# Kernel tuning notes

Hardware: AMD Instinct MI355X
Metric: run time of the kernel (lower is better)

Reference implementation:

```python
import jax, jax.numpy as jnp
import numpy as np

HIDDEN = 4096
N_HEADS = 32
N_KV_HEADS = 8
HEAD_DIM = HIDDEN // N_HEADS  # 128
Q_BITS = 8
ROPE_BASE = 10000.0


def setup_inputs() -> dict:
    key = jax.random.key(0)
    ks = jax.random.split(key, 6)
    b, s = 1, 2048
    hidden_states = jax.random.normal(ks[0], (b, s, HIDDEN), dtype=jnp.float32)
    position_ids = jnp.arange(s, dtype=jnp.int64 if jax.config.jax_enable_x64 else jnp.int32)[None, :]
    w_scale = 0.02
    wq = jax.random.normal(ks[1], (N_HEADS * HEAD_DIM, HIDDEN), dtype=jnp.float32) * w_scale
    wk = jax.random.normal(ks[2], (N_KV_HEADS * HEAD_DIM, HIDDEN), dtype=jnp.float32) * w_scale
    wv = jax.random.normal(ks[3], (N_KV_HEADS * HEAD_DIM, HIDDEN), dtype=jnp.float32) * w_scale
    wo = jax.random.normal(ks[4], (HIDDEN, N_HEADS * HEAD_DIM), dtype=jnp.float32) * w_scale
    return {"hidden_states": hidden_states, "wq": wq, "wk": wk, "wv": wv, "wo": wo,
            "position_ids": position_ids}


def _rope_tables(seq_len):
    inv_freq = 1.0 / (ROPE_BASE ** (jnp.arange(0, HEAD_DIM, 2, dtype=jnp.float32) / HEAD_DIM))
    t = jnp.arange(seq_len, dtype=jnp.float32)
    freqs = jnp.einsum('i,j->ij', t, inv_freq)          # [s, hd/2]
    emb = jnp.concatenate([freqs, freqs], axis=-1)      # [s, hd]
    return jnp.cos(emb), jnp.sin(emb)


def _rotate_half(x):
    x1, x2 = x[..., :HEAD_DIM // 2], x[..., HEAD_DIM // 2:]
    return jnp.concatenate([-x2, x1], axis=-1)


def _sym_quant_dequant(x):
    # per-token symmetric int8 quantization along head_dim (sym_quant + sym_dequant)
    q_max = 2 ** (Q_BITS - 1) - 1
    scale = jnp.clip(jnp.max(jnp.abs(x), axis=-1, keepdims=True) / q_max, 1e-9, None)
    q_int = jnp.clip(jnp.round(x / scale), -(q_max + 1), q_max)
    return q_int * scale


def reference(hidden_states, wq, wk, wv, wo, position_ids):
    b, s, _ = hidden_states.shape
    # projections -> [b, n_heads, s, head_dim]
    q = (hidden_states @ wq.T).reshape(b, s, N_HEADS, HEAD_DIM).transpose(0, 2, 1, 3)
    k = (hidden_states @ wk.T).reshape(b, s, N_KV_HEADS, HEAD_DIM).transpose(0, 2, 1, 3)
    v = (hidden_states @ wv.T).reshape(b, s, N_KV_HEADS, HEAD_DIM).transpose(0, 2, 1, 3)

    cos, sin = _rope_tables(s)
    cos = cos[position_ids][:, None]  # [b, 1, s, hd]
    sin = sin[position_ids][:, None]
    q = q * cos + _rotate_half(q) * sin
    k = k * cos + _rotate_half(k) * sin

    # int8 symmetric quantize/dequantize of K and V (KV-cache quantization)
    k = _sym_quant_dequant(k)
    v = _sym_quant_dequant(v)

    # GQA repeat_kv: [b, n_kv, s, hd] -> [b, n_heads, s, hd]
    n_rep = N_HEADS // N_KV_HEADS
    k = jnp.repeat(k, n_rep, axis=1)
    v = jnp.repeat(v, n_rep, axis=1)

    scores = jnp.einsum('bhqd,bhkd->bhqk', q, k) / jnp.sqrt(jnp.float32(HEAD_DIM))
    causal = jnp.tril(jnp.ones((s, s), dtype=bool))
    scores = jnp.where(causal, scores, jnp.float32(-1e9))
    attn = jax.nn.softmax(scores, axis=-1)

    out = jnp.einsum('bhqk,bhkd->bhqd', attn, v)
    out = out.transpose(0, 2, 1, 3).reshape(b, s, N_HEADS * HEAD_DIM)
    return out @ wo.T
```

## Files before the change

### kernel.cpp

```cpp
#include <hip/hip_runtime.h>


#define S_LEN 2048
#define HID 4096
#define NH 32
#define NKV 8
#define HD 128
#define QKV_N 6144

typedef __bf16 bf16x8 __attribute__((ext_vector_type(8)));
typedef float f32x4 __attribute__((ext_vector_type(4)));

__device__ __forceinline__ unsigned short f2b(float f) {
  unsigned int u = __float_as_uint(f);
  u += 0x7fffu + ((u >> 16) & 1u);
  return (unsigned short)(u >> 16);
}
__device__ __forceinline__ float b2f(unsigned short h) {
  return __uint_as_float(((unsigned int)h) << 16);
}
__device__ __forceinline__ void gl_lds16(const void* g, void* l) {
  __builtin_amdgcn_global_load_lds(
      (__attribute__((address_space(1))) void*)g,
      (__attribute__((address_space(3))) void*)l, 16, 0, 0);
}
__device__ __forceinline__ bf16x8 ds_read128(const void* p) {
  bf16x8 r;
  unsigned a = (unsigned)(unsigned long long)
      (__attribute__((address_space(3))) const void*)p;
  asm volatile("ds_read_b128 %0, %1" : "=v"(r) : "v"(a));
  return r;
}
__device__ __forceinline__ int swz(int row) {
  return ((row & 7) << 4) ^ (((row >> 3) & 1) << 5);
}
__device__ __forceinline__ void barrier_np() {
  asm volatile("" ::: "memory");
  __builtin_amdgcn_s_barrier();
  asm volatile("" ::: "memory");
}

__global__ __launch_bounds__(256) void cast_kernel(const float* __restrict__ src,
                                                   unsigned short* __restrict__ dst,
                                                   int n4) {
  int i = blockIdx.x * 256 + threadIdx.x;
  if (i >= n4) return;
  float4 v = ((const float4*)src)[i];
  ushort4 o;
  o.x = f2b(v.x); o.y = f2b(v.y); o.z = f2b(v.z); o.w = f2b(v.w);
  ((ushort4*)dst)[i] = o;
}

template <int OUT_BF16>
__global__ __launch_bounds__(512, 2) void gemm_bt(const unsigned short* __restrict__ A,
                                                  const unsigned short* __restrict__ B,
                                                  void* __restrict__ Cout,
                                                  int M, int N, int K) {
  __shared__ __align__(16) char lds[131072];
  const int tid = threadIdx.x;
  const int lane = tid & 63, wave = tid >> 6;
  const int quad = lane >> 4, l16 = lane & 15;
  const int wave_m = wave >> 2, wave_n = wave & 3;
  const long row0 = (long)blockIdx.y * 256;
  const long col0 = (long)blockIdx.x * 256;
  const int NT = K >> 6;
  const long rowstride = (long)K * 2;

  f32x4 acc[8][4] = {};

  auto stage = [&](const unsigned short* G, long base0, int ob, int T, int h, int tbuf) {
    if (T >= NT) return;
    char* dst = lds + tbuf * 65536 + ob + h * 16384 + wave * 1024;
    const char* src = (const char*)G + (base0 + h * 128) * rowstride + (long)T * 128;
#pragma unroll
    for (int c = 0; c < 2; ++c) {
      int b = c * 8192 + wave * 1024 + lane * 16;
      int r = b >> 7, cb = b & 127;
      gl_lds16(src + (long)r * rowstride + (cb ^ swz(r)), dst + c * 8192);
    }
  };

#define STAGE_A(T, h, tbuf) stage(A, row0, 0, (T), (h), (tbuf))
#define STAGE_B(T, h, tbuf) stage(B, col0, 32768, (T), (h), (tbuf))

  auto readA = [&](const char* base, bf16x8 (&a)[2][4]) {
#pragma unroll
    for (int mi = 0; mi < 4; ++mi) {
      int r = wave_m * 64 + mi * 16 + l16;
      const char* rp = base + r * 128;
      int sw = swz(r);
      a[0][mi] = ds_read128(rp + ((quad * 16) ^ sw));
      a[1][mi] = ds_read128(rp + ((64 + quad * 16) ^ sw));
    }
  };
  auto readB = [&](const char* base, bf16x8 (&b)[2][2]) {
#pragma unroll
    for (int ni = 0; ni < 2; ++ni) {
      int r = wave_n * 32 + ni * 16 + l16;
      const char* rp = base + r * 128;
      int sw = swz(r);
      b[0][ni] = ds_read128(rp + ((quad * 16) ^ sw));
      b[1][ni] = ds_read128(rp + ((64 + quad * 16) ^ sw));
    }
  };

#define WAITL0                                            \
  do {                                                    \
    asm volatile("s_waitcnt lgkmcnt(0)" ::: "memory");    \
    __builtin_amdgcn_sched_barrier(0);                    \
  } while (0)

#define MFMA_BLOCK(MH, NHh, A_, B_)                                          \
  do {                                                                       \
    __builtin_amdgcn_s_setprio(1);                                           \
    _Pragma("unroll")                                                        \
    for (int ks = 0; ks < 2; ++ks)                                           \
      _Pragma("unroll")                                                      \
      for (int mi = 0; mi < 4; ++mi)                                         \
        _Pragma("unroll")                                                    \
        for (int ni = 0; ni < 2; ++ni)                                       \
          acc[(MH) * 4 + mi][(NHh) * 2 + ni] =                               \
              __builtin_amdgcn_mfma_f32_16x16x32_bf16(                       \
                  A_[ks][mi], B_[ks][ni],                                    \
                  acc[(MH) * 4 + mi][(NHh) * 2 + ni], 0, 0, 0);              \
    __builtin_amdgcn_s_setprio(0);                                           \
  } while (0)

  STAGE_A(0, 0, 0); STAGE_B(0, 0, 0); STAGE_A(0, 1, 0); STAGE_B(0, 1, 0);
  STAGE_A(1, 0, 1); STAGE_B(1, 0, 1);
  asm volatile("s_waitcnt vmcnt(4)" ::: "memory");
  barrier_np();

  for (int g = 0; g < NT; ++g) {
    const int buf = g & 1;
    const char* Ab = lds + buf * 65536;
    const char* Bb = Ab + 32768;
    bf16x8 a[2][4], b0[2][2], b1[2][2];

    readA(Ab, a);
    readB(Bb, b0);
    STAGE_A(g + 1, 1, buf ^ 1);
    barrier_np();
    WAITL0;
    MFMA_BLOCK(0, 0, a, b0);
    barrier_np();

    readB(Bb + 16384, b1);
    STAGE_B(g + 1, 1, buf ^ 1);
    barrier_np();
    WAITL0;
    MFMA_BLOCK(0, 1, a, b1);
    barrier_np();

    readA(Ab + 16384, a);
    STAGE_A(g + 2, 0, buf);
    barrier_np();
    WAITL0;
    MFMA_BLOCK(1, 0, a, b0);
    barrier_np();

    STAGE_B(g + 2, 0, buf);
    barrier_np();
    WAITL0;
    MFMA_BLOCK(1, 1, a, b1);
    if (g + 2 < NT) { asm volatile("s_waitcnt vmcnt(4)" ::: "memory"); }
    else            { asm volatile("s_waitcnt vmcnt(0)" ::: "memory"); }
    barrier_np();
  }
#undef STAGE_A
#undef STAGE_B
#undef WAITL0
#undef MFMA_BLOCK

#pragma unroll
  for (int mi = 0; mi < 8; ++mi) {
    const int mh = mi >> 2, mq = mi & 3;
#pragma unroll
    for (int ni = 0; ni < 4; ++ni) {
      const int nh = ni >> 1, nq = ni & 1;
#pragma unroll
      for (int r = 0; r < 4; ++r) {
        long row = row0 + mh * 128 + wave_m * 64 + mq * 16 + quad * 4 + r;
        long col = col0 + nh * 128 + wave_n * 32 + nq * 16 + l16;
        float v = acc[mi][ni][r];
        if (OUT_BF16) ((unsigned short*)Cout)[row * N + col] = f2b(v);
        else          ((float*)Cout)[row * N + col] = v;
      }
    }
  }
}

__global__ __launch_bounds__(256) void postproc(const unsigned short* __restrict__ qkv,
                                                const int* __restrict__ pos_ids,
                                                unsigned short* __restrict__ Qb,
                                                unsigned short* __restrict__ Kb,
                                                unsigned short* __restrict__ Vb) {
  const int s = blockIdx.x;
  const int lane = threadIdx.x & 63, wave = threadIdx.x >> 6;
  const float pos = (float)pos_ids[s];
  const float invf = expf(-(float)lane * 0.14391156831212787f);
  const float ang = pos * invf;
  const float ca = cosf(ang), sa = sinf(ang);

  for (int r = wave; r < 48; r += 4) {
    if (r < 32) {
      const unsigned short* src = qkv + (long)s * QKV_N + r * HD;
      float x0 = b2f(src[lane]), x1 = b2f(src[lane + 64]);
      unsigned short* dst = Qb + ((long)r * S_LEN + s) * HD;
      dst[lane]      = f2b(x0 * ca - x1 * sa);
      dst[lane + 64] = f2b(x1 * ca + x0 * sa);
    } else if (r < 40) {
      int h = r - 32;
      const unsigned short* src = qkv + (long)s * QKV_N + 4096 + h * HD;
      float x0 = b2f(src[lane]), x1 = b2f(src[lane + 64]);
      float y0 = x0 * ca - x1 * sa;
      float y1 = x1 * ca + x0 * sa;
      float m = fmaxf(fabsf(y0), fabsf(y1));
      for (int off = 32; off; off >>= 1) m = fmaxf(m, __shfl_xor(m, off, 64));
      float scale = fmaxf(m / 127.0f, 1e-9f);
      float q0 = fminf(fmaxf(rintf(y0 / scale), -128.f), 127.f);
      float q1 = fminf(fmaxf(rintf(y1 / scale), -128.f), 127.f);
      unsigned short* dst = Kb + ((long)h * S_LEN + s) * HD;
      dst[lane]      = f2b(q0 * scale);
      dst[lane + 64] = f2b(q1 * scale);
    } else {
      int h = r - 40;
      const unsigned short* src = qkv + (long)s * QKV_N + 5120 + h * HD;
      float x0 = b2f(src[lane]), x1 = b2f(src[lane + 64]);
      float m = fmaxf(fabsf(x0), fabsf(x1));
      for (int off = 32; off; off >>= 1) m = fmaxf(m, __shfl_xor(m, off, 64));
      float scale = fmaxf(m / 127.0f, 1e-9f);
      float q0 = fminf(fmaxf(rintf(x0 / scale), -128.f), 127.f);
      float q1 = fminf(fmaxf(rintf(x1 / scale), -128.f), 127.f);
      unsigned short* dst = Vb + ((long)h * S_LEN + s) * HD;
      dst[lane]      = f2b(q0 * scale);
      dst[lane + 64] = f2b(q1 * scale);
    }
  }
}

__global__ __launch_bounds__(256) void transpose_v(const unsigned short* __restrict__ Vb,
                                                   unsigned short* __restrict__ Vtb) {
  __shared__ unsigned short t[64][136];
  const int h = blockIdx.x >> 5, st = blockIdx.x & 31;
  const int tid = threadIdx.x;
  const long vbase = (long)h * S_LEN * HD;
#pragma unroll
  for (int p = 0; p < 8; ++p) {
    int e = p * 1024 + tid * 4;
    int sl = e >> 7, d = e & 127;
    ushort4 v = *(const ushort4*)(Vb + vbase + (long)(st * 64 + sl) * HD + d);
    t[sl][d] = v.x; t[sl][d + 1] = v.y; t[sl][d + 2] = v.z; t[sl][d + 3] = v.w;
  }
  __syncthreads();
  const long tbase = (long)h * HD * S_LEN;
#pragma unroll
  for (int p = 0; p < 8; ++p) {
    int o = p * 1024 + tid * 4;
    int d = o >> 6, sl = o & 63;
    ushort4 v;
    v.x = t[sl][d]; v.y = t[sl + 1][d]; v.z = t[sl + 2][d]; v.w = t[sl + 3][d];
    *(ushort4*)(Vtb + tbase + (long)d * S_LEN + st * 64 + sl) = v;
  }
}

__global__ __launch_bounds__(256, 2) void attn_kernel(const unsigned short* __restrict__ Qb,
                                                      const unsigned short* __restrict__ Kb,
                                                      const unsigned short* __restrict__ Vtb,
                                                      unsigned short* __restrict__ Ob) {
  __shared__ __align__(16) char lds[81920];

  const int bx = blockIdx.x;
  const int p8 = bx & 1;
  const int g = (bx >> 1) & 7;
  const int b8 = bx >> 8;
  const int qt = (p8 ^ b8) ? (15 - g) : g;
  const int h = ((bx >> 4) & 15) + 16 * b8;
  const int hk = h >> 2;
  const int tid = threadIdx.x;
  const int lane = tid & 63, wave = tid >> 6;
  const int quad = lane >> 4, l16 = lane & 15;

  bf16x8 qf[2][4];
  {
    const unsigned short* qb =
        Qb + ((long)h * S_LEN + qt * 128 + wave * 32 + l16) * HD + quad * 8;
#pragma unroll
    for (int mi = 0; mi < 2; ++mi)
#pragma unroll
      for (int ks = 0; ks < 4; ++ks)
        qf[mi][ks] = *(const bf16x8*)(qb + mi * 16 * HD + ks * 32);
  }

  f32x4 O[2][8] = {};
  float mrow[2][4], lrow[2][4];
#pragma unroll
  for (int mi = 0; mi < 2; ++mi)
#pragma unroll
    for (int r = 0; r < 4; ++r) { mrow[mi][r] = -1e30f; lrow[mi][r] = 0.f; }

  const char* Kg = (const char*)(Kb + (long)hk * S_LEN * HD);
  const char* Vg = (const char*)(Vtb + (long)hk * HD * S_LEN);
  char* PsB = lds + 65536;
  const float sscale = 0.08838834764831845f;
  const int nsteps = 2 * qt + 2;

  auto stageK = [&](int step, int buf) {
    char* dst = lds + buf * 16384 + wave * 1024;
    const char* src = Kg + (long)step * 16384;
#pragma unroll
    for (int c = 0; c < 4; ++c) {
      int f = c * 4096 + tid * 16;
      int row = f >> 8, wb = f & 255;
      gl_lds16(src + row * 256 + (wb ^ swz(row)), dst + c * 4096);
    }
  };
  auto stageV = [&](int step, int buf) {
    char* dst = lds + 32768 + buf * 16384 + wave * 1024;
    const char* src = Vg + (long)step * 128;
#pragma unroll
    for (int c = 0; c < 4; ++c) {
      int f = c * 4096 + tid * 16;
      int d = f >> 7, wb = f & 127;
      gl_lds16(src + (long)d * (S_LEN * 2) + (wb ^ swz(d)), dst + c * 4096);
    }
  };

  stageK(0, 0);
  stageV(0, 0);

  for (int t = 0; t < nsteps; ++t) {
    __syncthreads();
    if (t + 1 < nsteps) {
      stageK(t + 1, (t + 1) & 1);
      stageV(t + 1, (t + 1) & 1);
    }
    const char* Ks = lds + (t & 1) * 16384;
    const char* Vs = lds + 32768 + (t & 1) * 16384;

    f32x4 S[2][4] = {};
    __builtin_amdgcn_s_setprio(1);
#pragma unroll
    for (int ni = 0; ni < 4; ++ni) {
      const int row = ni * 16 + l16;
      const char* kr = Ks + row * 256;
      const int sw = swz(row);
      const int q16 = quad * 16;
      bf16x8 kf0 = *(const bf16x8*)(kr + ((q16 + 0)   ^ sw));
      bf16x8 kf1 = *(const bf16x8*)(kr + ((q16 + 64)  ^ sw));
      bf16x8 kf2 = *(const bf16x8*)(kr + ((q16 + 128) ^ sw));
      bf16x8 kf3 = *(const bf16x8*)(kr + ((q16 + 192) ^ sw));
      S[0][ni] = __builtin_amdgcn_mfma_f32_16x16x32_bf16(qf[0][0], kf0, S[0][ni], 0, 0, 0);
      S[1][ni] = __builtin_amdgcn_mfma_f32_16x16x32_bf16(qf[1][0], kf0, S[1][ni], 0, 0, 0);
      S[0][ni] = __builtin_amdgcn_mfma_f32_16x16x32_bf16(qf[0][1], kf1, S[0][ni], 0, 0, 0);
      S[1][ni] = __builtin_amdgcn_mfma_f32_16x16x32_bf16(qf[1][1], kf1, S[1][ni], 0, 0, 0);
      S[0][ni] = __builtin_amdgcn_mfma_f32_16x16x32_bf16(qf[0][2], kf2, S[0][ni], 0, 0, 0);
      S[1][ni] = __builtin_amdgcn_mfma_f32_16x16x32_bf16(qf[1][2], kf2, S[1][ni], 0, 0, 0);
      S[0][ni] = __builtin_amdgcn_mfma_f32_16x16x32_bf16(qf[0][3], kf3, S[0][ni], 0, 0, 0);
      S[1][ni] = __builtin_amdgcn_mfma_f32_16x16x32_bf16(qf[1][3], kf3, S[1][ni], 0, 0, 0);
    }
    __builtin_amdgcn_s_setprio(0);

    const bool diag = (t >= 2 * qt);
    const int qrow_base = qt * 128 + wave * 32;
    float rmax[2][4];
#pragma unroll
    for (int mi = 0; mi < 2; ++mi)
#pragma unroll
      for (int r = 0; r < 4; ++r) rmax[mi][r] = -1e30f;
#pragma unroll
    for (int mi = 0; mi < 2; ++mi)
#pragma unroll
      for (int ni = 0; ni < 4; ++ni) {
        int col = t * 64 + ni * 16 + l16;
#pragma unroll
        for (int r = 0; r < 4; ++r) {
          int row = qrow_base + mi * 16 + quad * 4 + r;
          float v = S[mi][ni][r] * sscale;
          if (diag && col > row) v = -1e9f;
          S[mi][ni][r] = v;
          rmax[mi][r] = fmaxf(rmax[mi][r], v);
        }
      }
    float alpha[2][4], rsum[2][4];
#pragma unroll
    for (int mi = 0; mi < 2; ++mi)
#pragma unroll
      for (int r = 0; r < 4; ++r) {
        float v = rmax[mi][r];
        v = fmaxf(v, __shfl_xor(v, 1, 64));
        v = fmaxf(v, __shfl_xor(v, 2, 64));
        v = fmaxf(v, __shfl_xor(v, 4, 64));
        v = fmaxf(v, __shfl_xor(v, 8, 64));
        float mnew = fmaxf(mrow[mi][r], v);
        alpha[mi][r] = __expf(mrow[mi][r] - mnew);
        mrow[mi][r] = mnew;
        rsum[mi][r] = 0.f;
      }

#pragma unroll
    for (int mi = 0; mi < 2; ++mi)
#pragma unroll
      for (int ni = 0; ni < 4; ++ni)
#pragma unroll
        for (int r = 0; r < 4; ++r) {
          float p = __expf(S[mi][ni][r] - mrow[mi][r]);
          rsum[mi][r] += p;
          int prow = wave * 32 + mi * 16 + quad * 4 + r;
          int pcol2 = (ni * 16 + l16) * 2;
          *(unsigned short*)(PsB + prow * 128 + (pcol2 ^ swz(prow))) = f2b(p);
        }
#pragma unroll
    for (int mi = 0; mi < 2; ++mi)
#pragma unroll
      for (int r = 0; r < 4; ++r) {
        float v = rsum[mi][r];
        v += __shfl_xor(v, 1, 64);
        v += __shfl_xor(v, 2, 64);
        v += __shfl_xor(v, 4, 64);
        v += __shfl_xor(v, 8, 64);
        lrow[mi][r] = lrow[mi][r] * alpha[mi][r] + v;
      }
#pragma unroll
    for (int mi = 0; mi < 2; ++mi)
#pragma unroll
      for (int ni = 0; ni < 8; ++ni)
#pragma unroll
        for (int r = 0; r < 4; ++r) O[mi][ni][r] *= alpha[mi][r];

    bf16x8 pf[2][2];
#pragma unroll
    for (int mi = 0; mi < 2; ++mi)
#pragma unroll
      for (int ks2 = 0; ks2 < 2; ++ks2) {
        int prow = wave * 32 + mi * 16 + l16;
        pf[mi][ks2] = *(const bf16x8*)(PsB + prow * 128 +
                                       ((ks2 * 64 + quad * 16) ^ swz(prow)));
      }
    __builtin_amdgcn_s_setprio(1);
#pragma unroll
    for (int ni = 0; ni < 8; ++ni) {
      const int row = ni * 16 + l16;
      const char* vr = Vs + row * 128;
      const int sw = swz(row);
      const int q16 = quad * 16;
      bf16x8 vf0 = *(const bf16x8*)(vr + ((q16 + 0)  ^ sw));
      bf16x8 vf1 = *(const bf16x8*)(vr + ((q16 + 64) ^ sw));
      O[0][ni] = __builtin_amdgcn_mfma_f32_16x16x32_bf16(pf[0][0], vf0, O[0][ni], 0, 0, 0);
      O[1][ni] = __builtin_amdgcn_mfma_f32_16x16x32_bf16(pf[1][0], vf0, O[1][ni], 0, 0, 0);
      O[0][ni] = __builtin_amdgcn_mfma_f32_16x16x32_bf16(pf[0][1], vf1, O[0][ni], 0, 0, 0);
      O[1][ni] = __builtin_amdgcn_mfma_f32_16x16x32_bf16(pf[1][1], vf1, O[1][ni], 0, 0, 0);
    }
    __builtin_amdgcn_s_setprio(0);
  }

#pragma unroll
  for (int mi = 0; mi < 2; ++mi)
#pragma unroll
    for (int r = 0; r < 4; ++r) {
      float inv = 1.0f / lrow[mi][r];
      long srow = qt * 128 + wave * 32 + mi * 16 + quad * 4 + r;
#pragma unroll
      for (int ni = 0; ni < 8; ++ni) {
        long col = (long)h * HD + ni * 16 + l16;
        Ob[srow * (long)HID + col] = f2b(O[mi][ni][r] * inv);
      }
    }
}

extern "C" void kernel_launch(void* const* d_in, const int* in_sizes, int n_in,
                              void* d_out, int out_size, void* d_ws, size_t ws_size,
                              hipStream_t stream) {
  const float* hidden = (const float*)d_in[0];
  const float* wq = (const float*)d_in[1];
  const float* wk = (const float*)d_in[2];
  const float* wv = (const float*)d_in[3];
  const float* wo = (const float*)d_in[4];
  const int* pos = (const int*)d_in[5];
  float* out = (float*)d_out;

  char* ws = (char*)d_ws;
  unsigned short* wqkv_b = (unsigned short*)(ws);
  unsigned short* wo_b   = (unsigned short*)(ws + 50331648);
  unsigned short* hid_b  = (unsigned short*)(ws + 83886080);
  unsigned short* qkv_b  = (unsigned short*)(ws + 100663296);
  unsigned short* Kb     = (unsigned short*)(ws + 125829120);
  unsigned short* Vb     = (unsigned short*)(ws + 130023424);
  unsigned short* Vtb    = (unsigned short*)(ws + 134217728);
  unsigned short* Qb     = hid_b;
  unsigned short* attn_b = qkv_b;

  cast_kernel<<<8388608 / 1024, 256, 0, stream>>>(hidden, hid_b, 8388608 / 4);
  cast_kernel<<<16777216 / 1024, 256, 0, stream>>>(wq, wqkv_b, 16777216 / 4);
  cast_kernel<<<4194304 / 1024, 256, 0, stream>>>(wk, wqkv_b + 16777216, 4194304 / 4);
  cast_kernel<<<4194304 / 1024, 256, 0, stream>>>(wv, wqkv_b + 20971520, 4194304 / 4);
  cast_kernel<<<16777216 / 1024, 256, 0, stream>>>(wo, wo_b, 16777216 / 4);

  gemm_bt<1><<<dim3(QKV_N / 256, S_LEN / 256), 512, 0, stream>>>(
      hid_b, wqkv_b, (void*)qkv_b, S_LEN, QKV_N, HID);

  postproc<<<S_LEN, 256, 0, stream>>>(qkv_b, pos, Qb, Kb, Vb);
  transpose_v<<<NKV * 32, 256, 0, stream>>>(Vb, Vtb);
  attn_kernel<<<NH * 16, 256, 0, stream>>>(Qb, Kb, Vtb, attn_b);

  gemm_bt<0><<<dim3(HID / 256, S_LEN / 256), 512, 0, stream>>>(
      attn_b, wo_b, (void*)out, S_LEN, HID, HID);
}
```

Before: 551.5 us.

## Split-K the output projection with atomics and restructure GEMM loop barriers

The output-projection GEMM is now split across two K halves in a third grid dimension. Each half accumulates into a zeroed fp32 output with atomicAdd, which raises the block count from 128 to 256 so more CUs are filled. The GEMM main loop is also reordered to issue all LDS reads and stages earlier, with fewer barriers and partial lgkmcnt waits. In exchange, the output needs a memset and the atomic traffic adds cost. The reduced barrier count may also risk LDS read/write hazards between buffers.

```diff
diff --git a/kernel.cpp b/kernel.cpp
--- a/kernel.cpp
+++ b/kernel.cpp
@@ -51,7 +51,7 @@
   ((ushort4*)dst)[i] = o;
 }
 
-template <int OUT_BF16>
+template <int CMODE, int SPLITK>
 __global__ __launch_bounds__(512, 2) void gemm_bt(const unsigned short* __restrict__ A,
                                                   const unsigned short* __restrict__ B,
                                                   void* __restrict__ Cout,
@@ -63,8 +63,11 @@
   const int wave_m = wave >> 2, wave_n = wave & 3;
   const long row0 = (long)blockIdx.y * 256;
   const long col0 = (long)blockIdx.x * 256;
-  const int NT = K >> 6;
+  const int Klen = K / SPLITK;
+  const int NT = Klen >> 6;
   const long rowstride = (long)K * 2;
+  const unsigned short* Ag = A + (long)blockIdx.z * Klen;
+  const unsigned short* Bg = B + (long)blockIdx.z * Klen;
 
   f32x4 acc[8][4] = {};
 
@@ -80,8 +83,8 @@
     }
   };
 
-#define STAGE_A(T, h, tbuf) stage(A, row0, 0, (T), (h), (tbuf))
-#define STAGE_B(T, h, tbuf) stage(B, col0, 32768, (T), (h), (tbuf))
+#define STAGE_A(T, h, tbuf) stage(Ag, row0, 0, (T), (h), (tbuf))
+#define STAGE_B(T, h, tbuf) stage(Bg, col0, 32768, (T), (h), (tbuf))
 
   auto readA = [&](const char* base, bf16x8 (&a)[2][4]) {
 #pragma unroll
@@ -104,10 +107,10 @@
     }
   };
 
-#define WAITL0                                            \
-  do {                                                    \
-    asm volatile("s_waitcnt lgkmcnt(0)" ::: "memory");    \
-    __builtin_amdgcn_sched_barrier(0);                    \
+#define WAITL(n)                                               \
+  do {                                                         \
+    asm volatile("s_waitcnt lgkmcnt(" #n ")" ::: "memory");    \
+    __builtin_amdgcn_sched_barrier(0);                         \
   } while (0)
 
 #define MFMA_BLOCK(MH, NHh, A_, B_)                                          \
@@ -129,7 +132,6 @@
   STAGE_A(0, 0, 0); STAGE_B(0, 0, 0); STAGE_A(0, 1, 0); STAGE_B(0, 1, 0);
   STAGE_A(1, 0, 1); STAGE_B(1, 0, 1);
   asm volatile("s_waitcnt vmcnt(4)" ::: "memory");
-  barrier_np();
 
   for (int g = 0; g < NT; ++g) {
     const int buf = g & 1;
@@ -137,39 +139,29 @@
     const char* Bb = Ab + 32768;
     bf16x8 a[2][4], b0[2][2], b1[2][2];
 
+    barrier_np();
     readA(Ab, a);
     readB(Bb, b0);
+    readB(Bb + 16384, b1);
     STAGE_A(g + 1, 1, buf ^ 1);
+    STAGE_B(g + 1, 1, buf ^ 1);
+    WAITL(4);
     barrier_np();
-    WAITL0;
+    STAGE_A(g + 2, 0, buf);
+    STAGE_B(g + 2, 0, buf);
     MFMA_BLOCK(0, 0, a, b0);
-    barrier_np();
-
-    readB(Bb + 16384, b1);
-    STAGE_B(g + 1, 1, buf ^ 1);
-    barrier_np();
-    WAITL0;
+    WAITL(0);
     MFMA_BLOCK(0, 1, a, b1);
-    barrier_np();
-
     readA(Ab + 16384, a);
-    STAGE_A(g + 2, 0, buf);
-    barrier_np();
-    WAITL0;
+    WAITL(0);
     MFMA_BLOCK(1, 0, a, b0);
-    barrier_np();
-
-    STAGE_B(g + 2, 0, buf);
-    barrier_np();
-    WAITL0;
     MFMA_BLOCK(1, 1, a, b1);
     if (g + 2 < NT) { asm volatile("s_waitcnt vmcnt(4)" ::: "memory"); }
     else            { asm volatile("s_waitcnt vmcnt(0)" ::: "memory"); }
-    barrier_np();
   }
 #undef STAGE_A
 #undef STAGE_B
-#undef WAITL0
+#undef WAITL
 #undef MFMA_BLOCK
 
 #pragma unroll
@@ -183,8 +175,9 @@
         long row = row0 + mh * 128 + wave_m * 64 + mq * 16 + quad * 4 + r;
         long col = col0 + nh * 128 + wave_n * 32 + nq * 16 + l16;
         float v = acc[mi][ni][r];
-        if (OUT_BF16) ((unsigned short*)Cout)[row * N + col] = f2b(v);
-        else          ((float*)Cout)[row * N + col] = v;
+        if (CMODE == 1)      ((unsigned short*)Cout)[row * N + col] = f2b(v);
+        else if (CMODE == 2) atomicAdd((float*)Cout + row * N + col, v);
+        else                 ((float*)Cout)[row * N + col] = v;
       }
     }
   }
@@ -496,13 +489,14 @@
   cast_kernel<<<4194304 / 1024, 256, 0, stream>>>(wv, wqkv_b + 20971520, 4194304 / 4);
   cast_kernel<<<16777216 / 1024, 256, 0, stream>>>(wo, wo_b, 16777216 / 4);
 
-  gemm_bt<1><<<dim3(QKV_N / 256, S_LEN / 256), 512, 0, stream>>>(
+  gemm_bt<1, 1><<<dim3(QKV_N / 256, S_LEN / 256), 512, 0, stream>>>(
       hid_b, wqkv_b, (void*)qkv_b, S_LEN, QKV_N, HID);
 
   postproc<<<S_LEN, 256, 0, stream>>>(qkv_b, pos, Qb, Kb, Vb);
   transpose_v<<<NKV * 32, 256, 0, stream>>>(Vb, Vtb);
   attn_kernel<<<NH * 16, 256, 0, stream>>>(Qb, Kb, Vtb, attn_b);
 
-  gemm_bt<0><<<dim3(HID / 256, S_LEN / 256), 512, 0, stream>>>(
+  hipMemsetAsync(out, 0, (size_t)S_LEN * HID * 4, stream);
+  gemm_bt<2, 2><<<dim3(HID / 256, S_LEN / 256, 2), 512, 0, stream>>>(
       attn_b, wo_b, (void*)out, S_LEN, HID, HID);
 }
```

Result: no change. 551.1 us (-0.1%).
